# Kernel tuning notes

Hardware: AMD Instinct MI355X
Metric: run time of the kernel (lower is better)

Reference implementation:

```python
import jax, jax.numpy as jnp
import numpy as np

N_NODES = 20000
N_EDGES = 160000
FEAT = 512
HEADS = 4
NEG_SLOPE = 0.2


def setup_inputs() -> dict:
    key = jax.random.key(0)
    ks = jax.random.split(key, 8)
    s = 1.0 / np.sqrt(FEAT)
    return {
        "x": jax.random.normal(ks[0], (N_NODES, FEAT), dtype=jnp.float32),
        "edge_index": jax.random.randint(ks[1], (2, N_EDGES), 0, N_NODES, dtype=jnp.int32),
        "W_l": jax.random.normal(ks[2], (FEAT, HEADS * FEAT), dtype=jnp.float32) * s,
        "W_r": jax.random.normal(ks[3], (FEAT, HEADS * FEAT), dtype=jnp.float32) * s,
        "att": jax.random.normal(ks[4], (HEADS, FEAT), dtype=jnp.float32) * s,
        "bias": jax.random.normal(ks[5], (FEAT,), dtype=jnp.float32) * 0.01,
        "W_cls": jax.random.normal(ks[6], (FEAT, 2), dtype=jnp.float32) * s,
        "b_cls": jnp.zeros((2,), dtype=jnp.float32),
    }


def reference(x, edge_index, W_l, W_r, att, bias, W_cls, b_cls):
    N = x.shape[0]
    H, C = att.shape
    # PyG GATv2Conv default: add self-loops
    loops = jnp.arange(N, dtype=edge_index.dtype)
    ei = jnp.concatenate([edge_index, jnp.stack([loops, loops])], axis=1)
    src, dst = ei[0], ei[1]  # message j -> i

    xl = (x @ W_l).reshape(N, H, C)  # source transform
    xr = (x @ W_r).reshape(N, H, C)  # target transform

    # GATv2 score: e_ij = att . LeakyReLU(xl_j + xr_i)   -> [E, H]
    u = xl[src] + xr[dst]                      # [E, H, C]
    e = jnp.einsum('ehc,hc->eh', jax.nn.leaky_relu(u, NEG_SLOPE), att)

    # segment softmax over incoming edges of each dst node
    m = jax.ops.segment_max(e, dst, num_segments=N)          # [N, H]
    alpha = jnp.exp(e - m[dst])
    denom = jax.ops.segment_sum(alpha, dst, num_segments=N)  # [N, H]
    alpha = alpha / denom[dst]

    # aggregate: out_i = sum_j alpha_ij * xl_j
    out = jax.ops.segment_sum(alpha[:, :, None] * xl[src], dst, num_segments=N)  # [N,H,C]
    out = out.mean(axis=1) + bias  # concat=False -> mean over heads, then bias

    return out @ W_cls + b_cls  # [N, num_classes]
```

## Files before the change

### kernel.cpp

```cpp
#include <hip/hip_runtime.h>
#include <hip/hip_bf16.h>

#define FEAT    512
#define HEADS   4
#define NEG     0.2f

typedef unsigned int uint;
typedef unsigned short ushort_t;
typedef __attribute__((ext_vector_type(8))) short bf16x8v;
typedef __attribute__((ext_vector_type(4))) float f32x4v;
typedef __attribute__((address_space(3))) uint lds_u32_t;
typedef __attribute__((address_space(1))) const uint g_u32_t;

__device__ inline float bf2f(ushort_t h) { return __uint_as_float(((uint)h) << 16); }
__device__ inline ushort_t f2bf(float f) {
    uint u = __float_as_uint(f);
    u += 0x7fff + ((u >> 16) & 1);
    return (ushort_t)(u >> 16);
}
__device__ inline float2 up2(uint d) {
    return make_float2(__uint_as_float(d << 16), __uint_as_float(d & 0xffff0000u));
}
__device__ inline float2 f2add(float2 a, float2 b) { return make_float2(a.x + b.x, a.y + b.y); }
__device__ inline float2 f2min0(float2 a) { return make_float2(fminf(a.x, 0.f), fminf(a.y, 0.f)); }
__device__ inline float2 f2fma(float2 a, float2 b, float2 c) {
    return make_float2(fmaf(a.x, b.x, c.x), fmaf(a.y, b.y, c.y));
}
__device__ inline float2 f2fmas(float s, float2 b, float2 c) {
    return make_float2(fmaf(s, b.x, c.x), fmaf(s, b.y, c.y));
}

__global__ void probe_dtype(const ushort_t* __restrict__ x, int* flag) {
    int lane = threadIdx.x;
    int hits = 0;
    for (int i = lane; i < 128; i += 64) {
        ushort_t w = x[2 * i];
        uint hb = (w >> 8) & 0x7f;
        hits += (hb >= 0x38 && hb <= 0x42) ? 1 : 0;
    }
    #pragma unroll
    for (int off = 32; off >= 1; off >>= 1) hits += __shfl_xor(hits, off);
    if (lane == 0) *flag = (hits >= 64) ? 1 : 0;
}

__global__ __launch_bounds__(256) void canon_kernel(const void* __restrict__ in,
                                                    ushort_t* __restrict__ outp,
                                                    const int* __restrict__ flag, long long n) {
    long long i0 = ((long long)blockIdx.x * 256 + threadIdx.x) * 8;
    if (i0 + 8 <= n) {
        if (*flag) {
            *(uint4*)&outp[i0] = *(const uint4*)((const ushort_t*)in + i0);
        } else {
            const float* f = (const float*)in + i0;
            float4 a = *(const float4*)f, b = *(const float4*)(f + 4);
            ushort_t o[8] = {f2bf(a.x), f2bf(a.y), f2bf(a.z), f2bf(a.w),
                             f2bf(b.x), f2bf(b.y), f2bf(b.z), f2bf(b.w)};
            *(uint4*)&outp[i0] = *(uint4*)o;
        }
    } else {
        for (long long i = i0; i < n; ++i)
            outp[i] = (*flag) ? ((const ushort_t*)in)[i] : f2bf(((const float*)in)[i]);
    }
}

__global__ void init_deg_kernel(int* deg, int N) {
    int i = blockIdx.x * blockDim.x + threadIdx.x;
    if (i < N) deg[i] = 1;
}

__global__ void hist_kernel(const int* __restrict__ dst, int* deg, int E, int N) {
    int i = blockIdx.x * blockDim.x + threadIdx.x;
    if (i < E) {
        int d = dst[i];
        if ((uint)d < (uint)N) atomicAdd(&deg[d], 1);
    }
}

__global__ __launch_bounds__(256) void scan1(const int* __restrict__ deg, int* __restrict__ part,
                                             int* __restrict__ bsum, int N) {
    __shared__ int tmp[256];
    int b = blockIdx.x, tid = threadIdx.x;
    int i0 = b * 1024 + tid * 4;
    int v[4] = {0, 0, 0, 0};
    if (i0 + 4 <= N) { int4 q = *(const int4*)&deg[i0]; v[0]=q.x; v[1]=q.y; v[2]=q.z; v[3]=q.w; }
    else { for (int j = 0; j < 4; ++j) v[j] = (i0 + j < N) ? deg[i0 + j] : 0; }
    int s0 = v[0], s1 = s0 + v[1], s2 = s1 + v[2], s3 = s2 + v[3];
    tmp[tid] = s3;
    __syncthreads();
    for (int off = 1; off < 256; off <<= 1) {
        int t = (tid >= off) ? tmp[tid - off] : 0;
        __syncthreads();
        tmp[tid] += t;
        __syncthreads();
    }
    int base = tid ? tmp[tid - 1] : 0;
    int e[4] = {base, base + s0, base + s1, base + s2};
    if (i0 + 4 <= N) { *(int4*)&part[i0] = make_int4(e[0], e[1], e[2], e[3]); }
    else { for (int j = 0; j < 4; ++j) if (i0 + j < N) part[i0 + j] = e[j]; }
    if (tid == 255) bsum[b] = tmp[255];
}

__global__ void scan2(int* __restrict__ bsum, int* __restrict__ offsN, int Nb) {
    int lane = threadIdx.x;
    int carry = 0;
    for (int base = 0; base < Nb; base += 64) {
        int idx = base + lane;
        int v = (idx < Nb) ? bsum[idx] : 0;
        int incl = v;
        #pragma unroll
        for (int off = 1; off < 64; off <<= 1) {
            int t = __shfl_up(incl, off);
            if (lane >= off) incl += t;
        }
        if (idx < Nb) bsum[idx] = carry + (incl - v);
        carry += __shfl(incl, 63);
    }
    if (lane == 0) *offsN = carry;
}

__global__ __launch_bounds__(256) void scan3(const int* __restrict__ part, const int* __restrict__ bsum,
                                             int* __restrict__ offsets, int* __restrict__ cursor, int N) {
    int b = blockIdx.x;
    int add = bsum[b];
    int i0 = b * 1024 + threadIdx.x * 4;
    #pragma unroll
    for (int j = 0; j < 4; ++j) {
        int i = i0 + j;
        if (i < N) { int o = part[i] + add; offsets[i] = o; cursor[i] = o; }
    }
}

__global__ void scatter_kernel(const int* __restrict__ src, const int* __restrict__ dst,
                               int* cursor, int* srcs, int E, int N) {
    int i = blockIdx.x * blockDim.x + threadIdx.x;
    if (i >= E + N) return;
    int s, d;
    if (i < E) { s = src[i]; d = dst[i]; }
    else       { s = i - E; d = i - E; }
    if ((uint)d >= (uint)N) return;
    int pos = atomicAdd(&cursor[d], 1);
    if ((uint)pos < (uint)(E + N)) srcs[pos] = s;
}

__global__ __launch_bounds__(256) void transpose_canon(const void* __restrict__ in,
                                                       ushort_t* __restrict__ outp,
                                                       const int* __restrict__ flag,
                                                       int K, int N) {
    __shared__ ushort_t t[64][72];
    int k0 = blockIdx.y * 64, n0 = blockIdx.x * 64;
    int tid = threadIdx.x;
    int r = tid >> 3;
    int c = (tid & 7) * 8;
    int isbf = *flag;
    #pragma unroll
    for (int p = 0; p < 2; ++p) {
        int row = r + p * 32;
        size_t base = (size_t)(k0 + row) * N + n0 + c;
        if (isbf) {
            *(uint4*)&t[row][c] = *(const uint4*)((const ushort_t*)in + base);
        } else {
            const float* f = (const float*)in + base;
            float4 a = *(const float4*)f, b = *(const float4*)(f + 4);
            ushort_t o[8] = {f2bf(a.x), f2bf(a.y), f2bf(a.z), f2bf(a.w),
                             f2bf(b.x), f2bf(b.y), f2bf(b.z), f2bf(b.w)};
            *(uint4*)&t[row][c] = *(uint4*)o;
        }
    }
    __syncthreads();
    #pragma unroll
    for (int p = 0; p < 2; ++p) {
        int row = r + p * 32;
        #pragma unroll
        for (int j = 0; j < 8; ++j)
            outp[(size_t)(n0 + row) * K + k0 + c + j] = t[c + j][row];
    }
}

__global__ __launch_bounds__(256) void gemm128(const ushort_t* __restrict__ A,
                                               const ushort_t* __restrict__ Bt,
                                               ushort_t* __restrict__ C,
                                               int M, int Nn, int K) {
    __shared__ ushort_t As[128 * 32];
    __shared__ ushort_t Bs[128 * 32];
    int tid = threadIdx.x;
    int wave = tid >> 6, lane = tid & 63;
    int row0 = blockIdx.y * 128, col0 = blockIdx.x * 128;
    int wm = (wave >> 1) * 64, wn = (wave & 1) * 64;

    f32x4v acc[4][4];
    #pragma unroll
    for (int i = 0; i < 4; ++i)
        #pragma unroll
        for (int j = 0; j < 4; ++j) acc[i][j] = (f32x4v){0.f, 0.f, 0.f, 0.f};

    int fm = lane & 15, kqi = lane >> 4;
    int kqs = kqi ^ (fm >> 2);

    const ushort_t* srcA[2];
    const ushort_t* srcB[2];
    ushort_t* dstA[2];
    ushort_t* dstB[2];
    #pragma unroll
    for (int i = 0; i < 2; ++i) {
        int p = (wave * 2 + i) * 64 + lane;
        int row = p >> 2;
        int kp = (p & 3) ^ ((row >> 2) & 3);
        int gra = row0 + row; if (gra >= M) gra = M - 1;
        srcA[i] = &A[(size_t)gra * K + kp * 8];
        srcB[i] = &Bt[(size_t)(col0 + row) * K + kp * 8];
        dstA[i] = &As[p * 8];
        dstB[i] = &Bs[p * 8];
    }

    for (int k0 = 0; k0 < K; k0 += 32) {
        #pragma unroll
        for (int i = 0; i < 2; ++i) {
            __builtin_amdgcn_global_load_lds((g_u32_t*)srcA[i], (lds_u32_t*)dstA[i], 16, 0, 0);
            __builtin_amdgcn_global_load_lds((g_u32_t*)srcB[i], (lds_u32_t*)dstB[i], 16, 0, 0);
            srcA[i] += 32; srcB[i] += 32;
        }
        __syncthreads();

        bf16x8v af[4], bfr[4];
        #pragma unroll
        for (int mi = 0; mi < 4; ++mi)
            af[mi] = *(const bf16x8v*)&As[(4 * (wm + mi * 16 + fm) + kqs) * 8];
        #pragma unroll
        for (int nj = 0; nj < 4; ++nj)
            bfr[nj] = *(const bf16x8v*)&Bs[(4 * (wn + nj * 16 + fm) + kqs) * 8];
        #pragma unroll
        for (int mi = 0; mi < 4; ++mi)
            #pragma unroll
            for (int nj = 0; nj < 4; ++nj)
                acc[mi][nj] = __builtin_amdgcn_mfma_f32_16x16x32_bf16(af[mi], bfr[nj], acc[mi][nj], 0, 0, 0);
        __syncthreads();
    }

    int col = lane & 15, rq = (lane >> 4) * 4;
    #pragma unroll
    for (int mi = 0; mi < 4; ++mi) {
        #pragma unroll
        for (int r = 0; r < 4; ++r) {
            int gm = row0 + wm + mi * 16 + rq + r;
            if (gm < M) {
                #pragma unroll
                for (int nj = 0; nj < 4; ++nj)
                    C[(size_t)gm * Nn + col0 + wn + nj * 16 + col] = f2bf(acc[mi][nj][r]);
            }
        }
    }
}

__global__ __launch_bounds__(256) void gat_aggregate(
    const ushort_t* __restrict__ xl, int xl_stride,
    const ushort_t* __restrict__ xr, int xr_stride,
    const int* __restrict__ offsets, const int* __restrict__ srcs,
    const ushort_t* __restrict__ att, const ushort_t* __restrict__ bias,
    const ushort_t* __restrict__ Wc, const ushort_t* __restrict__ bc,
    float* __restrict__ out, int c0, int Cn, int N, int EN) {
    int bn = blockIdx.x;
    if (bn >= Cn) return;
    int n = c0 + bn;
    int tid = threadIdx.x;
    int h = tid >> 6, lane = tid & 63;
    int hoff = h * FEAT + lane * 8;

    __shared__ float sh[HEADS][FEAT];
    __shared__ float r0s[HEADS], r1s[HEADS];

    float2 xrr[4], attr[4];
    { uint4 q = *(const uint4*)&xr[(size_t)bn * xr_stride + hoff];
      xrr[0] = up2(q.x); xrr[1] = up2(q.y); xrr[2] = up2(q.z); xrr[3] = up2(q.w); }
    { uint4 q = *(const uint4*)&att[hoff];
      attr[0] = up2(q.x); attr[1] = up2(q.y); attr[2] = up2(q.z); attr[3] = up2(q.w); }

    int start = offsets[n], end = offsets[n + 1];
    start = max(0, min(start, EN));
    end   = max(start, min(end, EN));
    int deg = end - start;

    int sv = 0;
    if (lane < deg) sv = srcs[start + lane];

    float l = 0.f;
    float2 acc[4] = {{0.f,0.f},{0.f,0.f},{0.f,0.f},{0.f,0.f}};
    const ushort_t* xlh = xl + hoff;
    const float2 cneg = make_float2(NEG - 1.0f, NEG - 1.0f);

    auto body = [&](uint4 q) {
        float2 v[4] = {up2(q.x), up2(q.y), up2(q.z), up2(q.w)};
        float2 p2 = make_float2(0.f, 0.f);
        #pragma unroll
        for (int j = 0; j < 4; ++j) {
            float2 u  = f2add(v[j], xrr[j]);
            float2 lr = f2fma(f2min0(u), cneg, u);
            p2 = f2fma(lr, attr[j], p2);
        }
        float p = p2.x + p2.y;
        #pragma unroll
        for (int off = 32; off >= 1; off >>= 1) p += __shfl_xor(p, off);
        float w = __expf(p);
        l += w;
        #pragma unroll
        for (int j = 0; j < 4; ++j) acc[j] = f2fmas(w, v[j], acc[j]);
    };

    int e = 0;
    for (; e + 2 <= deg; e += 2) {
        int s0 = (e < 64) ? __shfl(sv, e) : srcs[start + e];
        int s1 = (e + 1 < 64) ? __shfl(sv, e + 1) : srcs[start + e + 1];
        if ((uint)s0 >= (uint)N) s0 = 0;
        if ((uint)s1 >= (uint)N) s1 = 0;
        uint4 q0 = *(const uint4*)(xlh + (size_t)s0 * xl_stride);
        uint4 q1 = *(const uint4*)(xlh + (size_t)s1 * xl_stride);
        body(q0);
        body(q1);
    }
    if (e < deg) {
        int s0 = (e < 64) ? __shfl(sv, e) : srcs[start + e];
        if ((uint)s0 >= (uint)N) s0 = 0;
        body(*(const uint4*)(xlh + (size_t)s0 * xl_stride));
    }

    float inv = 0.25f / fmaxf(l, 1e-35f);
    #pragma unroll
    for (int j = 0; j < 4; ++j) {
        sh[h][lane * 8 + 2 * j]     = acc[j].x * inv;
        sh[h][lane * 8 + 2 * j + 1] = acc[j].y * inv;
    }
    __syncthreads();

    float p0 = 0.f, p1 = 0.f;
    for (int c = tid; c < FEAT; c += 256) {
        float f = sh[0][c] + sh[1][c] + sh[2][c] + sh[3][c] + bf2f(bias[c]);
        uint w2 = *(const uint*)&Wc[c * 2];
        p0 = fmaf(f, bf2f((ushort_t)(w2 & 0xffff)), p0);
        p1 = fmaf(f, bf2f((ushort_t)(w2 >> 16)), p1);
    }
    #pragma unroll
    for (int off = 32; off >= 1; off >>= 1) {
        p0 += __shfl_xor(p0, off);
        p1 += __shfl_xor(p1, off);
    }
    if (lane == 0) { r0s[h] = p0; r1s[h] = p1; }
    __syncthreads();
    if (tid == 0) {
        out[(size_t)n * 2 + 0] = r0s[0] + r0s[1] + r0s[2] + r0s[3] + bf2f(bc[0]);
        out[(size_t)n * 2 + 1] = r1s[0] + r1s[1] + r1s[2] + r1s[3] + bf2f(bc[1]);
    }
}

extern "C" void kernel_launch(void* const* d_in, const int* in_sizes, int n_in,
                              void* d_out, int out_size, void* d_ws, size_t ws_size,
                              hipStream_t stream) {
    const void* x    = d_in[0];
    const int*  ei   = (const int*)d_in[1];
    const void* W_l  = d_in[2];
    const void* W_r  = d_in[3];
    const void* att  = d_in[4];
    const void* bias = d_in[5];
    const void* Wc   = d_in[6];
    const void* bc   = d_in[7];
    float* out = (float*)d_out;

    const int N  = in_sizes[0] / FEAT;
    const int E  = in_sizes[1] / 2;
    const int K  = FEAT;
    const int HC = HEADS * FEAT;
    const int EN = E + N;
    const int Nb = (N + 1023) / 1024;

    const int* src = ei;
    const int* dst = ei + E;

    char* base = (char*)d_ws;
    size_t off = 0;
    auto alloc = [&](size_t bytes) -> char* {
        char* p = base + off;
        off = (off + bytes + 255) & ~(size_t)255;
        return p;
    };
    int* flag    = (int*)alloc(4);
    int* offsets = (int*)alloc((size_t)(N + 1) * 4);
    int* cursor  = (int*)alloc((size_t)N * 4);
    int* deg     = (int*)alloc((size_t)N * 4);
    int* part    = (int*)alloc((size_t)N * 4);
    int* bsum    = (int*)alloc((size_t)(Nb + 1) * 4);
    int* srcs    = (int*)alloc((size_t)EN * 4);
    ushort_t* attc  = (ushort_t*)alloc((size_t)HC * 2);
    ushort_t* biasc = (ushort_t*)alloc((size_t)FEAT * 2);
    ushort_t* Wcc   = (ushort_t*)alloc((size_t)FEAT * 2 * 2);
    ushort_t* bcc   = (ushort_t*)alloc(2 * 2);
    ushort_t* xc   = (ushort_t*)alloc((size_t)N * K * 2);
    ushort_t* Wcat = (ushort_t*)alloc((size_t)2 * HC * K * 2);
    size_t fixed = off;

    size_t need_merged = (size_t)N * 2 * HC * 2;
    bool merged = (ws_size >= fixed + need_merged);

    probe_dtype<<<1, 64, 0, stream>>>((const ushort_t*)x, flag);
    long long NX = (long long)N * K;
    canon_kernel<<<(int)((NX + 2047) / 2048), 256, 0, stream>>>(x, xc, flag, NX);
    canon_kernel<<<1, 256, 0, stream>>>(att, attc, flag, HC);
    canon_kernel<<<1, 256, 0, stream>>>(bias, biasc, flag, FEAT);
    canon_kernel<<<1, 256, 0, stream>>>(Wc, Wcc, flag, FEAT * 2);
    canon_kernel<<<1, 256, 0, stream>>>(bc, bcc, flag, 2);

    init_deg_kernel<<<(N + 255) / 256, 256, 0, stream>>>(deg, N);
    hist_kernel<<<(E + 255) / 256, 256, 0, stream>>>(dst, deg, E, N);
    scan1<<<Nb, 256, 0, stream>>>(deg, part, bsum, N);
    scan2<<<1, 64, 0, stream>>>(bsum, &offsets[N], Nb);
    scan3<<<Nb, 256, 0, stream>>>(part, bsum, offsets, cursor, N);
    scatter_kernel<<<(EN + 255) / 256, 256, 0, stream>>>(src, dst, cursor, srcs, E, N);

    dim3 tg(HC / 64, K / 64);
    transpose_canon<<<tg, 256, 0, stream>>>(W_l, Wcat, flag, K, HC);
    transpose_canon<<<tg, 256, 0, stream>>>(W_r, Wcat + (size_t)HC * K, flag, K, HC);

    if (merged) {
        ushort_t* xlr = (ushort_t*)(base + fixed);
        dim3 gg(2 * HC / 128, (N + 127) / 128);
        gemm128<<<gg, 256, 0, stream>>>(xc, Wcat, xlr, N, 2 * HC, K);
        gat_aggregate<<<N, 256, 0, stream>>>(xlr, 2 * HC, xlr + HC, 2 * HC,
                                             offsets, srcs, attc, biasc, Wcc, bcc,
                                             out, 0, N, N, EN);
    } else {
        ushort_t* xl = (ushort_t*)alloc((size_t)N * HC * 2);
        size_t remain = (ws_size > off) ? (ws_size - off) : 0;
        long long Cmax = (long long)(remain / ((size_t)HC * 2));
        int C = (Cmax >= N) ? N : (int)(Cmax & ~63LL);
        if (C < 64) C = 64;
        ushort_t* xrc = (ushort_t*)(base + off);
        ushort_t* Wlt = Wcat;
        ushort_t* Wrt = Wcat + (size_t)HC * K;

        dim3 gl(HC / 128, (N + 127) / 128);
        gemm128<<<gl, 256, 0, stream>>>(xc, Wlt, xl, N, HC, K);
        for (int c0 = 0; c0 < N; c0 += C) {
            int Cn = (N - c0 < C) ? (N - c0) : C;
            dim3 gr(HC / 128, (Cn + 127) / 128);
            gemm128<<<gr, 256, 0, stream>>>(xc + (size_t)c0 * K, Wrt, xrc, Cn, HC, K);
            gat_aggregate<<<Cn, 256, 0, stream>>>(xl, HC, xrc, HC,
                                                  offsets, srcs, attc, biasc, Wcc, bcc,
                                                  out, c0, Cn, N, EN);
        }
    }
}
```

Measured before the change: 368.7 us.

## Widen GEMM tile to 128x256 and drop LDS swizzle

The projection GEMM now computes a 128x256 output tile per block, with each wave owning 64x128 and holding 32 accumulators. This reuses each A fragment across eight B fragments, cutting LDS traffic and global loads per MFMA. The XOR swizzle on the LDS layout is also removed, which may bring back LDS bank conflicts. The larger accumulator set raises register pressure and halves the grid along N, which may lower occupancy.

```diff
diff --git a/kernel.cpp b/kernel.cpp
--- a/kernel.cpp
+++ b/kernel.cpp
@@ -176,39 +176,40 @@
     }
 }
 
-__global__ __launch_bounds__(256) void gemm128(const ushort_t* __restrict__ A,
-                                               const ushort_t* __restrict__ Bt,
-                                               ushort_t* __restrict__ C,
-                                               int M, int Nn, int K) {
+__global__ __launch_bounds__(256) void gemm_big(const ushort_t* __restrict__ A,
+                                                const ushort_t* __restrict__ Bt,
+                                                ushort_t* __restrict__ C,
+                                                int M, int Nn, int K) {
     __shared__ ushort_t As[128 * 32];
-    __shared__ ushort_t Bs[128 * 32];
+    __shared__ ushort_t Bs[256 * 32];
     int tid = threadIdx.x;
     int wave = tid >> 6, lane = tid & 63;
-    int row0 = blockIdx.y * 128, col0 = blockIdx.x * 128;
-    int wm = (wave >> 1) * 64, wn = (wave & 1) * 64;
-
-    f32x4v acc[4][4];
+    int row0 = blockIdx.y * 128, col0 = blockIdx.x * 256;
+    int wm = (wave >> 1) * 64, wn = (wave & 1) * 128;
+
+    f32x4v acc[4][8];
     #pragma unroll
     for (int i = 0; i < 4; ++i)
         #pragma unroll
-        for (int j = 0; j < 4; ++j) acc[i][j] = (f32x4v){0.f, 0.f, 0.f, 0.f};
-
-    int fm = lane & 15, kqi = lane >> 4;
-    int kqs = kqi ^ (fm >> 2);
-
-    const ushort_t* srcA[2];
-    const ushort_t* srcB[2];
-    ushort_t* dstA[2];
-    ushort_t* dstB[2];
+        for (int j = 0; j < 8; ++j) acc[i][j] = (f32x4v){0.f, 0.f, 0.f, 0.f};
+
+    int fm = lane & 15, kq8 = (lane >> 4) * 8;
+
+    const ushort_t* srcA[2]; ushort_t* dstA[2];
+    const ushort_t* srcB[4]; ushort_t* dstB[4];
     #pragma unroll
     for (int i = 0; i < 2; ++i) {
         int p = (wave * 2 + i) * 64 + lane;
-        int row = p >> 2;
-        int kp = (p & 3) ^ ((row >> 2) & 3);
+        int row = p >> 2, kp = p & 3;
         int gra = row0 + row; if (gra >= M) gra = M - 1;
         srcA[i] = &A[(size_t)gra * K + kp * 8];
+        dstA[i] = &As[p * 8];
+    }
+    #pragma unroll
+    for (int i = 0; i < 4; ++i) {
+        int p = (wave * 4 + i) * 64 + lane;
+        int row = p >> 2, kp = p & 3;
         srcB[i] = &Bt[(size_t)(col0 + row) * K + kp * 8];
-        dstA[i] = &As[p * 8];
         dstB[i] = &Bs[p * 8];
     }
 
@@ -216,23 +217,26 @@
         #pragma unroll
         for (int i = 0; i < 2; ++i) {
             __builtin_amdgcn_global_load_lds((g_u32_t*)srcA[i], (lds_u32_t*)dstA[i], 16, 0, 0);
+            srcA[i] += 32;
+        }
+        #pragma unroll
+        for (int i = 0; i < 4; ++i) {
             __builtin_amdgcn_global_load_lds((g_u32_t*)srcB[i], (lds_u32_t*)dstB[i], 16, 0, 0);
-            srcA[i] += 32; srcB[i] += 32;
+            srcB[i] += 32;
         }
         __syncthreads();
 
-        bf16x8v af[4], bfr[4];
-        #pragma unroll
-        for (int mi = 0; mi < 4; ++mi)
-            af[mi] = *(const bf16x8v*)&As[(4 * (wm + mi * 16 + fm) + kqs) * 8];
-        #pragma unroll
-        for (int nj = 0; nj < 4; ++nj)
-            bfr[nj] = *(const bf16x8v*)&Bs[(4 * (wn + nj * 16 + fm) + kqs) * 8];
-        #pragma unroll
-        for (int mi = 0; mi < 4; ++mi)
+        bf16x8v bfr[8];
+        #pragma unroll
+        for (int nj = 0; nj < 8; ++nj)
+            bfr[nj] = *(const bf16x8v*)&Bs[(wn + nj * 16 + fm) * 32 + kq8];
+        #pragma unroll
+        for (int mi = 0; mi < 4; ++mi) {
+            bf16x8v af = *(const bf16x8v*)&As[(wm + mi * 16 + fm) * 32 + kq8];
             #pragma unroll
-            for (int nj = 0; nj < 4; ++nj)
-                acc[mi][nj] = __builtin_amdgcn_mfma_f32_16x16x32_bf16(af[mi], bfr[nj], acc[mi][nj], 0, 0, 0);
+            for (int nj = 0; nj < 8; ++nj)
+                acc[mi][nj] = __builtin_amdgcn_mfma_f32_16x16x32_bf16(af, bfr[nj], acc[mi][nj], 0, 0, 0);
+        }
         __syncthreads();
     }
 
@@ -244,7 +248,7 @@
             int gm = row0 + wm + mi * 16 + rq + r;
             if (gm < M) {
                 #pragma unroll
-                for (int nj = 0; nj < 4; ++nj)
+                for (int nj = 0; nj < 8; ++nj)
                     C[(size_t)gm * Nn + col0 + wn + nj * 16 + col] = f2bf(acc[mi][nj][r]);
             }
         }
@@ -419,8 +423,8 @@
 
     if (merged) {
         ushort_t* xlr = (ushort_t*)(base + fixed);
-        dim3 gg(2 * HC / 128, (N + 127) / 128);
-        gemm128<<<gg, 256, 0, stream>>>(xc, Wcat, xlr, N, 2 * HC, K);
+        dim3 gg(2 * HC / 256, (N + 127) / 128);
+        gemm_big<<<gg, 256, 0, stream>>>(xc, Wcat, xlr, N, 2 * HC, K);
         gat_aggregate<<<N, 256, 0, stream>>>(xlr, 2 * HC, xlr + HC, 2 * HC,
                                              offsets, srcs, attc, biasc, Wcc, bcc,
                                              out, 0, N, N, EN);
@@ -434,12 +438,12 @@
         ushort_t* Wlt = Wcat;
         ushort_t* Wrt = Wcat + (size_t)HC * K;
 
-        dim3 gl(HC / 128, (N + 127) / 128);
-        gemm128<<<gl, 256, 0, stream>>>(xc, Wlt, xl, N, HC, K);
+        dim3 gl(HC / 256, (N + 127) / 128);
+        gemm_big<<<gl, 256, 0, stream>>>(xc, Wlt, xl, N, HC, K);
         for (int c0 = 0; c0 < N; c0 += C) {
             int Cn = (N - c0 < C) ? (N - c0) : C;
-            dim3 gr(HC / 128, (Cn + 127) / 128);
-            gemm128<<<gr, 256, 0, stream>>>(xc + (size_t)c0 * K, Wrt, xrc, Cn, HC, K);
+            dim3 gr(HC / 256, (Cn + 127) / 128);
+            gemm_big<<<gr, 256, 0, stream>>>(xc + (size_t)c0 * K, Wrt, xrc, Cn, HC, K);
             gat_aggregate<<<Cn, 256, 0, stream>>>(xl, HC, xrc, HC,
                                                   offsets, srcs, attc, biasc, Wcc, bcc,
                                                   out, c0, Cn, N, EN);
```

Result: slower. 462.7 us (+25.5%).
